# Performance work log

Hardware: AMD Instinct MI355X
Metric: run time of the kernel (lower is better)

The kernel has to match this reference:

```python
import jax, jax.numpy as jnp
import numpy as np

N_HEAD = 16
HEAD_DIM = 64
ROPE_BASE = 10000.0


def _rope_cos_sin(T, dtype):
    # inv_freq: [HEAD_DIM/2]
    inv_freq = 1.0 / (ROPE_BASE ** (jnp.arange(0, HEAD_DIM, 2, dtype=jnp.float32) / HEAD_DIM))
    t = jnp.arange(T, dtype=jnp.float32)
    freqs = jnp.einsum('i,j->ij', t, inv_freq)          # [T, D/2]
    emb = jnp.concatenate([freqs, freqs], axis=-1)       # [T, D]
    return jnp.cos(emb).astype(dtype), jnp.sin(emb).astype(dtype)


def _rotate_half(x):
    x1, x2 = jnp.split(x, 2, axis=-1)
    return jnp.concatenate([-x2, x1], axis=-1)


def setup_inputs() -> dict:
    key = jax.random.key(0)
    k1, k2, k3, k4 = jax.random.split(key, 4)
    B, T, C = 4, 2048, N_HEAD * HEAD_DIM
    s = 1.0 / np.sqrt(C)
    return {
        'x': jax.random.normal(k1, (B, T, C), dtype=jnp.float32),
        'Wq': jax.random.normal(k2, (C, C), dtype=jnp.float32) * s,
        'Wkv': jax.random.normal(k3, (C, 2 * C), dtype=jnp.float32) * s,
        'Wc': jax.random.normal(k4, (C, C), dtype=jnp.float32) * s,
    }


def reference(x, Wq, Wkv, Wc):
    B, T, C = x.shape
    H, D = N_HEAD, HEAD_DIM

    q = x @ Wq                                   # [B,T,C]
    kv = x @ Wkv                                 # [B,T,2C]
    k, v = jnp.split(kv, 2, axis=-1)

    # [B,T,C] -> [B,H,T,D]
    def to_heads(t):
        return t.reshape(B, T, H, D).transpose(0, 2, 1, 3)
    q, k, v = to_heads(q), to_heads(k), to_heads(v)

    cos, sin = _rope_cos_sin(T, x.dtype)         # [T,D] each
    cos = cos[None, None]                        # [1,1,T,D]
    sin = sin[None, None]
    q = q * cos + _rotate_half(q) * sin
    k = k * cos + _rotate_half(k) * sin

    scale = 1.0 / np.sqrt(D)
    scores = jnp.einsum('bhqd,bhkd->bhqk', q, k) * scale   # [B,H,T,T]
    causal = jnp.tril(jnp.ones((T, T), dtype=bool))
    scores = jnp.where(causal, scores, jnp.finfo(scores.dtype).min)
    attn = jax.nn.softmax(scores, axis=-1)
    y = jnp.einsum('bhqk,bhkd->bhqd', attn, v)   # [B,H,T,D]
    y = y.transpose(0, 2, 1, 3).reshape(B, T, C)
    return y @ Wc
```

## Files before the change

### kernel.cpp

```cpp
#include <hip/hip_runtime.h>
#include <math.h>

typedef __attribute__((ext_vector_type(4))) float f32x4;
typedef __attribute__((ext_vector_type(16))) float f32x16;
typedef __attribute__((ext_vector_type(8))) short bf16x8;
typedef __attribute__((ext_vector_type(4))) unsigned short us4;
typedef __attribute__((ext_vector_type(4))) unsigned int u32x4;

#define T_SEQ 2048
#define NH 16
#define HD 64
#define CDIM 1024

__device__ __forceinline__ unsigned short f2bf(float f) {
  unsigned int u = __float_as_uint(f);
  u += 0x7fffu + ((u >> 16) & 1u);
  return (unsigned short)(u >> 16);
}

__device__ __forceinline__ f32x16 zero16() {
  f32x16 z;
#pragma unroll
  for (int i = 0; i < 16; ++i) z[i] = 0.0f;
  return z;
}

#define GLOAD_LDS(g, l)                                                   \
  __builtin_amdgcn_global_load_lds(                                       \
      (const __attribute__((address_space(1))) unsigned int*)(g),         \
      (__attribute__((address_space(3))) unsigned int*)(l), 16, 0, 0)

__global__ __launch_bounds__(256) void cast_x_kernel(const float* __restrict__ src,
                                                     unsigned short* __restrict__ dst,
                                                     int n4) {
  int i = blockIdx.x * 256 + threadIdx.x;
  if (i >= n4) return;
  f32x4 v = reinterpret_cast<const f32x4*>(src)[i];
  us4 o;
#pragma unroll
  for (int j = 0; j < 4; ++j) o[j] = f2bf(v[j]);
  reinterpret_cast<us4*>(dst)[i] = o;
}

__global__ __launch_bounds__(256) void transpose_cast_kernel(const float* __restrict__ src,
                                                             unsigned short* __restrict__ dst,
                                                             int ldsrc, int lddst) {
  __shared__ float tile[32][33];
  int n0 = blockIdx.x * 32, k0 = blockIdx.y * 32;
  int tx = threadIdx.x, ty = threadIdx.y;
#pragma unroll
  for (int r = 0; r < 4; ++r)
    tile[ty + r * 8][tx] = src[(size_t)(k0 + ty + r * 8) * ldsrc + n0 + tx];
  __syncthreads();
#pragma unroll
  for (int r = 0; r < 4; ++r)
    dst[(size_t)(n0 + ty + r * 8) * lddst + k0 + tx] = f2bf(tile[tx][ty + r * 8]);
}

__global__ __launch_bounds__(256) void rope_table_kernel(float* __restrict__ cost,
                                                         float* __restrict__ sint) {
  int idx = blockIdx.x * 256 + threadIdx.x;
  int t = idx >> 5, j = idx & 31;
  double invf = pow(10000.0, -(double)j / 32.0);
  double ang = (double)t * invf;
  cost[idx] = (float)cos(ang);
  sint[idx] = (float)sin(ang);
}

template <int MODE>
__global__ __launch_bounds__(256) void gemm_kernel(
    const unsigned short* __restrict__ A, const unsigned short* __restrict__ Bt,
    int M, int N, int K,
    unsigned short* __restrict__ qo, unsigned short* __restrict__ ko,
    unsigned short* __restrict__ vTo, const float* __restrict__ cost,
    const float* __restrict__ sint, float* __restrict__ out) {
  __shared__ __align__(16) unsigned short As[2][128 * 64];
  __shared__ __align__(16) unsigned short Bs[2][128 * 64];
  const int tid = threadIdx.x;
  const int lane = tid & 63;
  const int wave = tid >> 6;
  const int wr = wave >> 1, wc = wave & 1;
  const int m0 = blockIdx.y * 128, n0 = blockIdx.x * 128;
  const int lrow = lane & 15, lhi = lane >> 4;
  const int srow = lane >> 3;
  const int scol = (((lane & 7) ^ srow) * 8);

  f32x4 zero4 = {0.f, 0.f, 0.f, 0.f};
  f32x4 acc[4][4];
#pragma unroll
  for (int mi = 0; mi < 4; ++mi)
#pragma unroll
    for (int ni = 0; ni < 4; ++ni) acc[mi][ni] = zero4;

  const int ntiles = K >> 6;
  auto stage = [&](int bf, int kt) {
#pragma unroll
    for (int c2 = 0; c2 < 4; ++c2) {
      const int c = wave * 4 + c2;
      GLOAD_LDS(&A[(size_t)(m0 + c * 8 + srow) * K + kt + scol], &As[bf][c * 512]);
      GLOAD_LDS(&Bt[(size_t)(n0 + c * 8 + srow) * K + kt + scol], &Bs[bf][c * 512]);
    }
  };

  stage(0, 0);
  __syncthreads();
  int cur = 0;
  for (int ti = 0; ti < ntiles; ++ti) {
    if (ti + 1 < ntiles) stage(cur ^ 1, (ti + 1) * 64);
#pragma unroll
    for (int kk = 0; kk < 2; ++kk) {
      bf16x8 af[4], bfv[4];
#pragma unroll
      for (int i = 0; i < 4; ++i) {
        const int ra = wr * 64 + i * 16 + lrow;
        const int rb = wc * 64 + i * 16 + lrow;
        const int cba = (kk * 4 + lhi) ^ (ra & 7);
        const int cbb = (kk * 4 + lhi) ^ (rb & 7);
        af[i] = *reinterpret_cast<const bf16x8*>(&As[cur][ra * 64 + cba * 8]);
        bfv[i] = *reinterpret_cast<const bf16x8*>(&Bs[cur][rb * 64 + cbb * 8]);
      }
#pragma unroll
      for (int mi = 0; mi < 4; ++mi)
#pragma unroll
        for (int ni = 0; ni < 4; ++ni)
          acc[mi][ni] =
              __builtin_amdgcn_mfma_f32_16x16x32_bf16(af[mi], bfv[ni], acc[mi][ni], 0, 0, 0);
    }
    __syncthreads();
    cur ^= 1;
  }

  if (MODE == 0) {
#pragma unroll
    for (int mi = 0; mi < 4; ++mi)
#pragma unroll
      for (int ni = 0; ni < 4; ++ni) {
        int n = n0 + wc * 64 + ni * 16 + lrow;
#pragma unroll
        for (int r = 0; r < 4; ++r) {
          int m = m0 + wr * 64 + mi * 16 + lhi * 4 + r;
          out[(size_t)m * N + n] = acc[mi][ni][r];
        }
      }
  } else {
#pragma unroll
    for (int mi = 0; mi < 4; ++mi) {
      int mb = m0 + wr * 64 + mi * 16 + lhi * 4;
      int b = mb >> 11, tb = mb & (T_SEQ - 1);
#pragma unroll
      for (int ni = 0; ni < 4; ++ni) {
        int n = n0 + wc * 64 + ni * 16 + lrow;
        int sec = n >> 10;
        int h = (n >> 6) & 15;
        int d = n & 63;
        int bh_ = b * NH + h;
        if (sec == 2) {
          int t64 = tb >> 6, ks = (tb >> 4) & 3, hiv = (tb >> 3) & 1, e0 = tb & 7;
          int dgrp = d >> 5, lanev = hiv * 32 + (d & 31);
          us4 pk;
#pragma unroll
          for (int r = 0; r < 4; ++r) pk[r] = f2bf(acc[mi][ni][r]);
          size_t addr =
              ((((size_t)bh_ * 32 + t64) * 2 + dgrp) * 4 + ks) * 512 + lanev * 8 + e0;
          *reinterpret_cast<us4*>(&vTo[addr]) = pk;
        } else {
          int dm = d & 31;
          float sgn = (d < 32) ? -1.0f : 1.0f;
          unsigned short* dstp = (sec == 0) ? qo : ko;
          int ks = d >> 4, hiq = (d >> 3) & 1, e = d & 7;
#pragma unroll
          for (int r = 0; r < 4; ++r) {
            int t = tb + r;
            float c = cost[t * 32 + dm], s = sint[t * 32 + dm];
            float val = acc[mi][ni][r] * c + sgn * acc[mi][ni ^ 2][r] * s;
            if (sec == 0) val *= 0.125f;
            int blk = t >> 5, lane_ = hiq * 32 + (t & 31);
            dstp[(((size_t)bh_ * 64 + blk) * 4 + ks) * 512 + lane_ * 8 + e] = f2bf(val);
          }
        }
      }
    }
  }
}

__global__ __launch_bounds__(256, 2) void attn_kernel(const unsigned short* __restrict__ qg,
                                                      const unsigned short* __restrict__ kg,
                                                      const unsigned short* __restrict__ vtg,
                                                      unsigned short* __restrict__ att) {
  const int tid = threadIdx.x;
  const int lane = tid & 63;
  const int w = tid >> 6;
  const int l31 = lane & 31, hi = lane >> 5;
  const int bid = (int)blockIdx.x;
  const int xcd = bid & 7, j = bid >> 3;
  const int bh = xcd * 8 + (j >> 3);
  const int p = (j & 7) * 4 + w;
  const unsigned short* qfp = qg + (size_t)bh * 131072;
  const unsigned short* kfp = kg + (size_t)bh * 131072;
  const unsigned short* vfp = vtg + (size_t)bh * 131072;
  const int b = bh >> 4, h = bh & 15;

  auto run_pos = [&](int pos) {
    const int qrow = pos * 32 + l31;
    bf16x8 qf[4];
#pragma unroll
    for (int ks = 0; ks < 4; ++ks)
      qf[ks] =
          *reinterpret_cast<const bf16x8*>(&qfp[((size_t)pos * 4 + ks) * 512 + lane * 8]);
    f32x16 oA = zero16(), oB = zero16();
    float mrun = -3.0e38f, lrun = 0.0f;
    const int myt = (pos >> 1) + 1;

    bf16x8 kA0[4], kB0[4], kA1[4], kB1[4];
    bf16x8 vA0[4], vB0[4], vA1[4], vB1[4];
#pragma unroll
    for (int ks = 0; ks < 4; ++ks) {
      kA0[ks] = *reinterpret_cast<const bf16x8*>(&kfp[(size_t)(0 + ks) * 512 + lane * 8]);
      kB0[ks] = *reinterpret_cast<const bf16x8*>(&kfp[(size_t)(4 + ks) * 512 + lane * 8]);
      vA0[ks] = *reinterpret_cast<const bf16x8*>(&vfp[(size_t)(0 + ks) * 512 + lane * 8]);
      vB0[ks] = *reinterpret_cast<const bf16x8*>(&vfp[(size_t)(4 + ks) * 512 + lane * 8]);
    }

    auto step = [&](int t, bf16x8 (&kcA)[4], bf16x8 (&kcB)[4], bf16x8 (&knA)[4],
                    bf16x8 (&knB)[4], bf16x8 (&vcA)[4], bf16x8 (&vcB)[4],
                    bf16x8 (&vnA)[4], bf16x8 (&vnB)[4]) {
      f32x16 sA = zero16(), sB = zero16();
      __builtin_amdgcn_s_setprio(1);
#pragma unroll
      for (int ks = 0; ks < 4; ++ks) {
        sA = __builtin_amdgcn_mfma_f32_32x32x16_bf16(kcA[ks], qf[ks], sA, 0, 0, 0);
        sB = __builtin_amdgcn_mfma_f32_32x32x16_bf16(kcB[ks], qf[ks], sB, 0, 0, 0);
      }
      __builtin_amdgcn_s_setprio(0);
      if (t + 1 < myt) {
#pragma unroll
        for (int ks = 0; ks < 4; ++ks) {
          knA[ks] = *reinterpret_cast<const bf16x8*>(
              &kfp[((size_t)(2 * t + 2) * 4 + ks) * 512 + lane * 8]);
          knB[ks] = *reinterpret_cast<const bf16x8*>(
              &kfp[((size_t)(2 * t + 3) * 4 + ks) * 512 + lane * 8]);
          vnA[ks] = *reinterpret_cast<const bf16x8*>(
              &vfp[((size_t)(2 * t + 2) * 4 + ks) * 512 + lane * 8]);
          vnB[ks] = *reinterpret_cast<const bf16x8*>(
              &vfp[((size_t)(2 * t + 3) * 4 + ks) * 512 + lane * 8]);
        }
      }
      if (t == myt - 1) {
        const int kvb = t * 64;
#pragma unroll
        for (int r = 0; r < 16; ++r) {
          int keyA = kvb + (r & 3) + 8 * (r >> 2) + 4 * hi;
          if (keyA > qrow) sA[r] = -1e30f;
          if (keyA + 32 > qrow) sB[r] = -1e30f;
        }
      }
      float tr[16];
#pragma unroll
      for (int i = 0; i < 16; ++i) tr[i] = fmaxf(sA[i], sB[i]);
#pragma unroll
      for (int i = 0; i < 8; ++i) tr[i] = fmaxf(tr[i], tr[i + 8]);
#pragma unroll
      for (int i = 0; i < 4; ++i) tr[i] = fmaxf(tr[i], tr[i + 4]);
      float tm = fmaxf(fmaxf(tr[0], tr[1]), fmaxf(tr[2], tr[3]));
      tm = fmaxf(tm, __shfl_xor(tm, 32));
      if (!__all(tm - mrun <= 8.0f)) {
        float mnew = fmaxf(mrun, tm);
        float alpha = __expf(mrun - mnew);
        lrun *= alpha;
#pragma unroll
        for (int i = 0; i < 16; ++i) {
          oA[i] *= alpha;
          oB[i] *= alpha;
        }
        mrun = mnew;
      }
#pragma unroll
      for (int i = 0; i < 16; ++i) {
        sA[i] = __expf(sA[i] - mrun);
        sB[i] = __expf(sB[i] - mrun);
      }
      float sr[16];
#pragma unroll
      for (int i = 0; i < 16; ++i) sr[i] = sA[i] + sB[i];
#pragma unroll
      for (int i = 0; i < 8; ++i) sr[i] += sr[i + 8];
#pragma unroll
      for (int i = 0; i < 4; ++i) sr[i] += sr[i + 4];
      float lsum = (sr[0] + sr[1]) + (sr[2] + sr[3]);
      lsum += __shfl_xor(lsum, 32);
      lrun += lsum;
      unsigned int ua[4], va[4], ub[4], vb[4];
#pragma unroll
      for (int m = 0; m < 4; ++m) {
        asm("v_cvt_pk_bf16_f32 %0, %1, %2" : "=v"(ua[m]) : "v"(sA[4 * m]), "v"(sA[4 * m + 1]));
        asm("v_cvt_pk_bf16_f32 %0, %1, %2" : "=v"(va[m]) : "v"(sA[4 * m + 2]), "v"(sA[4 * m + 3]));
        asm("v_cvt_pk_bf16_f32 %0, %1, %2" : "=v"(ub[m]) : "v"(sB[4 * m]), "v"(sB[4 * m + 1]));
        asm("v_cvt_pk_bf16_f32 %0, %1, %2" : "=v"(vb[m]) : "v"(sB[4 * m + 2]), "v"(sB[4 * m + 3]));
      }
      asm("v_permlane32_swap_b32 %0, %1" : "+v"(ua[0]), "+v"(ua[1]));
      asm("v_permlane32_swap_b32 %0, %1" : "+v"(va[0]), "+v"(va[1]));
      asm("v_permlane32_swap_b32 %0, %1" : "+v"(ua[2]), "+v"(ua[3]));
      asm("v_permlane32_swap_b32 %0, %1" : "+v"(va[2]), "+v"(va[3]));
      asm("v_permlane32_swap_b32 %0, %1" : "+v"(ub[0]), "+v"(ub[1]));
      asm("v_permlane32_swap_b32 %0, %1" : "+v"(vb[0]), "+v"(vb[1]));
      asm("v_permlane32_swap_b32 %0, %1" : "+v"(ub[2]), "+v"(ub[3]));
      asm("v_permlane32_swap_b32 %0, %1" : "+v"(vb[2]), "+v"(vb[3]));
      u32x4 w0 = {ua[0], va[0], ua[1], va[1]};
      u32x4 w1 = {ua[2], va[2], ua[3], va[3]};
      u32x4 w2 = {ub[0], vb[0], ub[1], vb[1]};
      u32x4 w3 = {ub[2], vb[2], ub[3], vb[3]};
      bf16x8 pf0 = __builtin_bit_cast(bf16x8, w0);
      bf16x8 pf1 = __builtin_bit_cast(bf16x8, w1);
      bf16x8 pf2 = __builtin_bit_cast(bf16x8, w2);
      bf16x8 pf3 = __builtin_bit_cast(bf16x8, w3);
      __builtin_amdgcn_s_setprio(1);
      oA = __builtin_amdgcn_mfma_f32_32x32x16_bf16(vcA[0], pf0, oA, 0, 0, 0);
      oB = __builtin_amdgcn_mfma_f32_32x32x16_bf16(vcB[0], pf0, oB, 0, 0, 0);
      oA = __builtin_amdgcn_mfma_f32_32x32x16_bf16(vcA[1], pf1, oA, 0, 0, 0);
      oB = __builtin_amdgcn_mfma_f32_32x32x16_bf16(vcB[1], pf1, oB, 0, 0, 0);
      oA = __builtin_amdgcn_mfma_f32_32x32x16_bf16(vcA[2], pf2, oA, 0, 0, 0);
      oB = __builtin_amdgcn_mfma_f32_32x32x16_bf16(vcB[2], pf2, oB, 0, 0, 0);
      oA = __builtin_amdgcn_mfma_f32_32x32x16_bf16(vcA[3], pf3, oA, 0, 0, 0);
      oB = __builtin_amdgcn_mfma_f32_32x32x16_bf16(vcB[3], pf3, oB, 0, 0, 0);
      __builtin_amdgcn_s_setprio(0);
    };

    int t = 0;
    while (t < myt) {
      step(t, kA0, kB0, kA1, kB1, vA0, vB0, vA1, vB1);
      ++t;
      if (t >= myt) break;
      step(t, kA1, kB1, kA0, kB0, vA1, vB1, vA0, vB0);
      ++t;
    }

    const float inv = 1.0f / lrun;
    const size_t obase = ((size_t)b * T_SEQ + qrow) * CDIM + h * HD;
#pragma unroll
    for (int g = 0; g < 4; ++g) {
      us4 pa, pb;
#pragma unroll
      for (int jj = 0; jj < 4; ++jj) {
        pa[jj] = f2bf(oA[4 * g + jj] * inv);
        pb[jj] = f2bf(oB[4 * g + jj] * inv);
      }
      *reinterpret_cast<us4*>(&att[obase + g * 8 + 4 * hi]) = pa;
      *reinterpret_cast<us4*>(&att[obase + 32 + g * 8 + 4 * hi]) = pb;
    }
  };

  run_pos(63 - p);
  run_pos(p);
}

extern "C" void kernel_launch(void* const* d_in, const int* in_sizes, int n_in,
                              void* d_out, int out_size, void* d_ws, size_t ws_size,
                              hipStream_t stream) {
  const float* x = (const float*)d_in[0];
  const float* Wq = (const float*)d_in[1];
  const float* Wkv = (const float*)d_in[2];
  const float* Wc = (const float*)d_in[3];
  float* out = (float*)d_out;

  char* ws = (char*)d_ws;
  size_t off = 0;
  auto alloc = [&](size_t bytes) {
    void* p = ws + off;
    off += (bytes + 255) & ~(size_t)255;
    return p;
  };
  const size_t NTOK = 4ull * T_SEQ;
  const size_t NELEM = NTOK * CDIM;
  unsigned short* xb = (unsigned short*)alloc(NELEM * 2);
  unsigned short* WT = (unsigned short*)alloc(3072ull * 1024 * 2);
  unsigned short* WcT = (unsigned short*)alloc(1024ull * 1024 * 2);
  unsigned short* qb = (unsigned short*)alloc(NELEM * 2);
  unsigned short* kb = (unsigned short*)alloc(NELEM * 2);
  unsigned short* vT = (unsigned short*)alloc(NELEM * 2);
  float* cost = (float*)alloc(T_SEQ * 32 * 4);
  float* sint = (float*)alloc(T_SEQ * 32 * 4);
  unsigned short* att = xb;

  cast_x_kernel<<<(int)(NELEM / 4 / 256), 256, 0, stream>>>(x, xb, (int)(NELEM / 4));
  transpose_cast_kernel<<<dim3(32, 32), dim3(32, 8), 0, stream>>>(Wq, WT, 1024, 1024);
  transpose_cast_kernel<<<dim3(64, 32), dim3(32, 8), 0, stream>>>(Wkv, WT + 1024 * 1024, 2048,
                                                                  1024);
  transpose_cast_kernel<<<dim3(32, 32), dim3(32, 8), 0, stream>>>(Wc, WcT, 1024, 1024);
  rope_table_kernel<<<T_SEQ * 32 / 256, 256, 0, stream>>>(cost, sint);

  gemm_kernel<1><<<dim3(3072 / 128, NTOK / 128), 256, 0, stream>>>(
      xb, WT, (int)NTOK, 3072, 1024, qb, kb, vT, cost, sint, nullptr);

  attn_kernel<<<dim3(512), 256, 0, stream>>>(qb, kb, vT, att);

  gemm_kernel<0><<<dim3(1024 / 128, NTOK / 128), 256, 0, stream>>>(
      att, WcT, (int)NTOK, 1024, 1024, nullptr, nullptr, nullptr, nullptr, nullptr, out);
}
```

Baseline: 174.2 us.

## Share K/V tiles across 8 waves via double-buffered LDS staging in attention

Restructures the attention kernel so each 512-thread block runs 8 waves, each owning one query position from a balanced pair of causal rows. K and V tiles are staged cooperatively into double-buffered shared memory with direct global-to-LDS loads, so all waves in the block reuse them. Before, each wave streamed K/V from global memory into its own registers. The change adds block-wide barriers every tile, and waves whose causal range ends early sit idle until the longest wave in the block finishes.

```diff
diff --git a/kernel.cpp b/kernel.cpp
--- a/kernel.cpp
+++ b/kernel.cpp
@@ -183,68 +183,61 @@
   }
 }
 
-__global__ __launch_bounds__(256, 2) void attn_kernel(const unsigned short* __restrict__ qg,
+__global__ __launch_bounds__(512, 2) void attn_kernel(const unsigned short* __restrict__ qg,
                                                       const unsigned short* __restrict__ kg,
                                                       const unsigned short* __restrict__ vtg,
                                                       unsigned short* __restrict__ att) {
+  __shared__ __align__(16) unsigned short Ks[2][4096];
+  __shared__ __align__(16) unsigned short Vs[2][4096];
   const int tid = threadIdx.x;
   const int lane = tid & 63;
   const int w = tid >> 6;
   const int l31 = lane & 31, hi = lane >> 5;
   const int bid = (int)blockIdx.x;
-  const int xcd = bid & 7, j = bid >> 3;
-  const int bh = xcd * 8 + (j >> 3);
-  const int p = (j & 7) * 4 + w;
+  const int second = bid >> 8;
+  const int q = bid & 255;
+  const int xcd = q & 7, g = q >> 3;
+  const int bh = xcd * 8 + (g >> 2);
+  const int ii = g & 3;
+  const int i = second ? (7 - ii) : ii;
+  const int pos = (w < 4) ? (4 * i + w) : (63 - 4 * i - (w - 4));
+  const int qrow = pos * 32 + l31;
+  const int myt = (pos >> 1) + 1;
+  const int maxT = 32 - 2 * i;
   const unsigned short* qfp = qg + (size_t)bh * 131072;
   const unsigned short* kfp = kg + (size_t)bh * 131072;
   const unsigned short* vfp = vtg + (size_t)bh * 131072;
   const int b = bh >> 4, h = bh & 15;
 
-  auto run_pos = [&](int pos) {
-    const int qrow = pos * 32 + l31;
-    bf16x8 qf[4];
-#pragma unroll
-    for (int ks = 0; ks < 4; ++ks)
-      qf[ks] =
-          *reinterpret_cast<const bf16x8*>(&qfp[((size_t)pos * 4 + ks) * 512 + lane * 8]);
-    f32x16 oA = zero16(), oB = zero16();
-    float mrun = -3.0e38f, lrun = 0.0f;
-    const int myt = (pos >> 1) + 1;
-
-    bf16x8 kA0[4], kB0[4], kA1[4], kB1[4];
-    bf16x8 vA0[4], vB0[4], vA1[4], vB1[4];
-#pragma unroll
-    for (int ks = 0; ks < 4; ++ks) {
-      kA0[ks] = *reinterpret_cast<const bf16x8*>(&kfp[(size_t)(0 + ks) * 512 + lane * 8]);
-      kB0[ks] = *reinterpret_cast<const bf16x8*>(&kfp[(size_t)(4 + ks) * 512 + lane * 8]);
-      vA0[ks] = *reinterpret_cast<const bf16x8*>(&vfp[(size_t)(0 + ks) * 512 + lane * 8]);
-      vB0[ks] = *reinterpret_cast<const bf16x8*>(&vfp[(size_t)(4 + ks) * 512 + lane * 8]);
-    }
-
-    auto step = [&](int t, bf16x8 (&kcA)[4], bf16x8 (&kcB)[4], bf16x8 (&knA)[4],
-                    bf16x8 (&knB)[4], bf16x8 (&vcA)[4], bf16x8 (&vcB)[4],
-                    bf16x8 (&vnA)[4], bf16x8 (&vnB)[4]) {
+  bf16x8 qf[4];
+#pragma unroll
+  for (int ks = 0; ks < 4; ++ks)
+    qf[ks] = *reinterpret_cast<const bf16x8*>(&qfp[((size_t)pos * 4 + ks) * 512 + lane * 8]);
+
+  f32x16 oA = zero16(), oB = zero16();
+  float mrun = -3.0e38f, lrun = 0.0f;
+
+  auto stage = [&](int bf, int t) {
+    GLOAD_LDS(&kfp[(size_t)t * 4096 + tid * 8], &Ks[bf][w * 512]);
+    GLOAD_LDS(&vfp[(size_t)t * 4096 + tid * 8], &Vs[bf][w * 512]);
+  };
+
+  stage(0, 0);
+  __syncthreads();
+  int buf = 0;
+  for (int t = 0; t < maxT; ++t) {
+    if (t + 1 < maxT) stage(buf ^ 1, t + 1);
+    if (t < myt) {
       f32x16 sA = zero16(), sB = zero16();
       __builtin_amdgcn_s_setprio(1);
 #pragma unroll
       for (int ks = 0; ks < 4; ++ks) {
-        sA = __builtin_amdgcn_mfma_f32_32x32x16_bf16(kcA[ks], qf[ks], sA, 0, 0, 0);
-        sB = __builtin_amdgcn_mfma_f32_32x32x16_bf16(kcB[ks], qf[ks], sB, 0, 0, 0);
+        bf16x8 ka = *reinterpret_cast<const bf16x8*>(&Ks[buf][ks * 512 + lane * 8]);
+        bf16x8 kb = *reinterpret_cast<const bf16x8*>(&Ks[buf][(4 + ks) * 512 + lane * 8]);
+        sA = __builtin_amdgcn_mfma_f32_32x32x16_bf16(ka, qf[ks], sA, 0, 0, 0);
+        sB = __builtin_amdgcn_mfma_f32_32x32x16_bf16(kb, qf[ks], sB, 0, 0, 0);
       }
       __builtin_amdgcn_s_setprio(0);
-      if (t + 1 < myt) {
-#pragma unroll
-        for (int ks = 0; ks < 4; ++ks) {
-          knA[ks] = *reinterpret_cast<const bf16x8*>(
-              &kfp[((size_t)(2 * t + 2) * 4 + ks) * 512 + lane * 8]);
-          knB[ks] = *reinterpret_cast<const bf16x8*>(
-              &kfp[((size_t)(2 * t + 3) * 4 + ks) * 512 + lane * 8]);
-          vnA[ks] = *reinterpret_cast<const bf16x8*>(
-              &vfp[((size_t)(2 * t + 2) * 4 + ks) * 512 + lane * 8]);
-          vnB[ks] = *reinterpret_cast<const bf16x8*>(
-              &vfp[((size_t)(2 * t + 3) * 4 + ks) * 512 + lane * 8]);
-        }
-      }
       if (t == myt - 1) {
         const int kvb = t * 64;
 #pragma unroll
@@ -256,11 +249,11 @@
       }
       float tr[16];
 #pragma unroll
-      for (int i = 0; i < 16; ++i) tr[i] = fmaxf(sA[i], sB[i]);
-#pragma unroll
-      for (int i = 0; i < 8; ++i) tr[i] = fmaxf(tr[i], tr[i + 8]);
-#pragma unroll
-      for (int i = 0; i < 4; ++i) tr[i] = fmaxf(tr[i], tr[i + 4]);
+      for (int k2 = 0; k2 < 16; ++k2) tr[k2] = fmaxf(sA[k2], sB[k2]);
+#pragma unroll
+      for (int k2 = 0; k2 < 8; ++k2) tr[k2] = fmaxf(tr[k2], tr[k2 + 8]);
+#pragma unroll
+      for (int k2 = 0; k2 < 4; ++k2) tr[k2] = fmaxf(tr[k2], tr[k2 + 4]);
       float tm = fmaxf(fmaxf(tr[0], tr[1]), fmaxf(tr[2], tr[3]));
       tm = fmaxf(tm, __shfl_xor(tm, 32));
       if (!__all(tm - mrun <= 8.0f)) {
@@ -268,24 +261,24 @@
         float alpha = __expf(mrun - mnew);
         lrun *= alpha;
 #pragma unroll
-        for (int i = 0; i < 16; ++i) {
-          oA[i] *= alpha;
-          oB[i] *= alpha;
+        for (int k2 = 0; k2 < 16; ++k2) {
+          oA[k2] *= alpha;
+          oB[k2] *= alpha;
         }
         mrun = mnew;
       }
 #pragma unroll
-      for (int i = 0; i < 16; ++i) {
-        sA[i] = __expf(sA[i] - mrun);
-        sB[i] = __expf(sB[i] - mrun);
+      for (int k2 = 0; k2 < 16; ++k2) {
+        sA[k2] = __expf(sA[k2] - mrun);
+        sB[k2] = __expf(sB[k2] - mrun);
       }
       float sr[16];
 #pragma unroll
-      for (int i = 0; i < 16; ++i) sr[i] = sA[i] + sB[i];
-#pragma unroll
-      for (int i = 0; i < 8; ++i) sr[i] += sr[i + 8];
-#pragma unroll
-      for (int i = 0; i < 4; ++i) sr[i] += sr[i + 4];
+      for (int k2 = 0; k2 < 16; ++k2) sr[k2] = sA[k2] + sB[k2];
+#pragma unroll
+      for (int k2 = 0; k2 < 8; ++k2) sr[k2] += sr[k2 + 8];
+#pragma unroll
+      for (int k2 = 0; k2 < 4; ++k2) sr[k2] += sr[k2 + 4];
       float lsum = (sr[0] + sr[1]) + (sr[2] + sr[3]);
       lsum += __shfl_xor(lsum, 32);
       lrun += lsum;
@@ -314,43 +307,43 @@
       bf16x8 pf2 = __builtin_bit_cast(bf16x8, w2);
       bf16x8 pf3 = __builtin_bit_cast(bf16x8, w3);
       __builtin_amdgcn_s_setprio(1);
-      oA = __builtin_amdgcn_mfma_f32_32x32x16_bf16(vcA[0], pf0, oA, 0, 0, 0);
-      oB = __builtin_amdgcn_mfma_f32_32x32x16_bf16(vcB[0], pf0, oB, 0, 0, 0);
-      oA = __builtin_amdgcn_mfma_f32_32x32x16_bf16(vcA[1], pf1, oA, 0, 0, 0);
-      oB = __builtin_amdgcn_mfma_f32_32x32x16_bf16(vcB[1], pf1, oB, 0, 0, 0);
-      oA = __builtin_amdgcn_mfma_f32_32x32x16_bf16(vcA[2], pf2, oA, 0, 0, 0);
-      oB = __builtin_amdgcn_mfma_f32_32x32x16_bf16(vcB[2], pf2, oB, 0, 0, 0);
-      oA = __builtin_amdgcn_mfma_f32_32x32x16_bf16(vcA[3], pf3, oA, 0, 0, 0);
-      oB = __builtin_amdgcn_mfma_f32_32x32x16_bf16(vcB[3], pf3, oB, 0, 0, 0);
+      {
+        bf16x8 v0 = *reinterpret_cast<const bf16x8*>(&Vs[buf][0 * 512 + lane * 8]);
+        bf16x8 v4 = *reinterpret_cast<const bf16x8*>(&Vs[buf][4 * 512 + lane * 8]);
+        oA = __builtin_amdgcn_mfma_f32_32x32x16_bf16(v0, pf0, oA, 0, 0, 0);
+        oB = __builtin_amdgcn_mfma_f32_32x32x16_bf16(v4, pf0, oB, 0, 0, 0);
+        bf16x8 v1 = *reinterpret_cast<const bf16x8*>(&Vs[buf][1 * 512 + lane * 8]);
+        bf16x8 v5 = *reinterpret_cast<const bf16x8*>(&Vs[buf][5 * 512 + lane * 8]);
+        oA = __builtin_amdgcn_mfma_f32_32x32x16_bf16(v1, pf1, oA, 0, 0, 0);
+        oB = __builtin_amdgcn_mfma_f32_32x32x16_bf16(v5, pf1, oB, 0, 0, 0);
+        bf16x8 v2 = *reinterpret_cast<const bf16x8*>(&Vs[buf][2 * 512 + lane * 8]);
+        bf16x8 v6 = *reinterpret_cast<const bf16x8*>(&Vs[buf][6 * 512 + lane * 8]);
+        oA = __builtin_amdgcn_mfma_f32_32x32x16_bf16(v2, pf2, oA, 0, 0, 0);
+        oB = __builtin_amdgcn_mfma_f32_32x32x16_bf16(v6, pf2, oB, 0, 0, 0);
+        bf16x8 v3 = *reinterpret_cast<const bf16x8*>(&Vs[buf][3 * 512 + lane * 8]);
+        bf16x8 v7 = *reinterpret_cast<const bf16x8*>(&Vs[buf][7 * 512 + lane * 8]);
+        oA = __builtin_amdgcn_mfma_f32_32x32x16_bf16(v3, pf3, oA, 0, 0, 0);
+        oB = __builtin_amdgcn_mfma_f32_32x32x16_bf16(v7, pf3, oB, 0, 0, 0);
+      }
       __builtin_amdgcn_s_setprio(0);
-    };
-
-    int t = 0;
-    while (t < myt) {
-      step(t, kA0, kB0, kA1, kB1, vA0, vB0, vA1, vB1);
-      ++t;
-      if (t >= myt) break;
-      step(t, kA1, kB1, kA0, kB0, vA1, vB1, vA0, vB0);
-      ++t;
-    }
-
-    const float inv = 1.0f / lrun;
-    const size_t obase = ((size_t)b * T_SEQ + qrow) * CDIM + h * HD;
-#pragma unroll
-    for (int g = 0; g < 4; ++g) {
-      us4 pa, pb;
-#pragma unroll
-      for (int jj = 0; jj < 4; ++jj) {
-        pa[jj] = f2bf(oA[4 * g + jj] * inv);
-        pb[jj] = f2bf(oB[4 * g + jj] * inv);
-      }
-      *reinterpret_cast<us4*>(&att[obase + g * 8 + 4 * hi]) = pa;
-      *reinterpret_cast<us4*>(&att[obase + 32 + g * 8 + 4 * hi]) = pb;
-    }
-  };
-
-  run_pos(63 - p);
-  run_pos(p);
+    }
+    __syncthreads();
+    buf ^= 1;
+  }
+
+  const float inv = 1.0f / lrun;
+  const size_t obase = ((size_t)b * T_SEQ + qrow) * CDIM + h * HD;
+#pragma unroll
+  for (int g2 = 0; g2 < 4; ++g2) {
+    us4 pa, pb;
+#pragma unroll
+    for (int jj = 0; jj < 4; ++jj) {
+      pa[jj] = f2bf(oA[4 * g2 + jj] * inv);
+      pb[jj] = f2bf(oB[4 * g2 + jj] * inv);
+    }
+    *reinterpret_cast<us4*>(&att[obase + g2 * 8 + 4 * hi]) = pa;
+    *reinterpret_cast<us4*>(&att[obase + 32 + g2 * 8 + 4 * hi]) = pb;
+  }
 }
 
 extern "C" void kernel_launch(void* const* d_in, const int* in_sizes, int n_in,
@@ -391,7 +384,7 @@
   gemm_kernel<1><<<dim3(3072 / 128, NTOK / 128), 256, 0, stream>>>(
       xb, WT, (int)NTOK, 3072, 1024, qb, kb, vT, cost, sint, nullptr);
 
-  attn_kernel<<<dim3(512), 256, 0, stream>>>(qb, kb, vT, att);
+  attn_kernel<<<dim3(512), 512, 0, stream>>>(qb, kb, vT, att);
 
   gemm_kernel<0><<<dim3(1024 / 128, NTOK / 128), 256, 0, stream>>>(
       att, WcT, (int)NTOK, 1024, 1024, nullptr, nullptr, nullptr, nullptr, nullptr, out);
```

New measurement: 170.4 us. 1.02x faster.
